# Performance work log

Hardware: AMD Instinct MI355X
Metric: run time of the kernel (lower is better)

## Reference

```python
import jax, jax.numpy as jnp
import numpy as np

# Static config matching init_kwargs
WZ, WH, WW = 2, 6, 12          # window size
MZ, MH, MW = 4, 16, 15          # ceil(input_shape / window_size) for (8,96,180)
HEADS, DIM, B = 6, 192, 1
DH = DIM // HEADS
P = WZ * WH * WW                # 144 tokens per window
WN = MZ * MH * MW               # 960 windows
WT = MZ * MH                    # 64 window types
SCALE = DH ** -0.5
TABLE = WZ * WZ * WH * WH * (2 * WW - 1)  # 3312 bias entries


def _position_index():
    zi = np.arange(WZ); zj = -np.arange(WZ) * WZ
    hi = np.arange(WH); hj = -np.arange(WH) * WH
    w = np.arange(WW)
    c1 = np.stack(np.meshgrid(zi, hi, w, indexing='ij')).reshape(3, -1)  # (3, P)
    c2 = np.stack(np.meshgrid(zj, hj, w, indexing='ij')).reshape(3, -1)  # (3, P)
    coords = (c1[:, :, None] - c2[:, None, :]).transpose(1, 2, 0)        # (P, P, 3)
    coords[:, :, 2] += WW - 1
    coords[:, :, 1] *= 2 * WW - 1
    coords[:, :, 0] *= (2 * WW - 1) * WH * WH
    return coords.sum(-1).reshape(-1)  # (P*P,)

POS_IDX = jnp.asarray(_position_index())


def setup_inputs() -> dict:
    key = jax.random.key(0)
    ks = jax.random.split(key, 5)
    x = jax.random.normal(ks[0], (B * WN, P, DIM), dtype=jnp.float32)
    mask = jnp.zeros((WN, P, P), dtype=jnp.float32)
    w_qkv = jax.random.normal(ks[1], (DIM, 3 * DIM), dtype=jnp.float32) * 0.02
    w_proj = jax.random.normal(ks[2], (DIM, DIM), dtype=jnp.float32) * 0.02
    b_proj = jnp.zeros((DIM,), dtype=jnp.float32)
    bias_table = jax.random.normal(ks[3], (TABLE, WT, HEADS), dtype=jnp.float32) * 0.02
    return {"x": x, "mask": mask, "w_qkv": w_qkv, "w_proj": w_proj,
            "b_proj": b_proj, "bias_table": bias_table}


def reference(x, mask, w_qkv, w_proj, b_proj, bias_table):
    BN = x.shape[0]  # B*WN
    qkv = (x @ w_qkv).reshape(BN, P, 3, HEADS, DH).transpose(2, 0, 3, 1, 4)  # (3,BN,h,P,dh)
    q, k, v = SCALE * qkv[0], qkv[1], qkv[2]
    attn = jnp.einsum('bhid,bhjd->bhij', q, k)  # (BN, h, P, P)
    # (B mZ mH mW) h P P -> (B mW) (mZ mH) h P P
    attn = attn.reshape(B, MZ, MH, MW, HEADS, P, P)
    attn = attn.transpose(0, 3, 1, 2, 4, 5, 6).reshape(B * MW, WT, HEADS, P, P)
    # gather earth-specific bias: (P*P, WT, h) -> (WT, h, P, P)
    bias = bias_table[POS_IDX].reshape(P, P, WT, HEADS).transpose(2, 3, 0, 1)
    attn = attn + bias  # broadcast over (B mW)
    # back to (B mZ mH mW) h P P
    attn = attn.reshape(B, MW, MZ, MH, HEADS, P, P)
    attn = attn.transpose(0, 2, 3, 1, 4, 5, 6).reshape(B, WN, HEADS, P, P)
    attn = attn + mask[None, :, None]  # (1, wN, 1, P, P)
    attn = jax.nn.softmax(attn, axis=-1).reshape(B * WN, HEADS, P, P)
    out = jnp.einsum('bhij,bhjd->bhid', attn, v)           # (BN, h, P, dh)
    out = out.transpose(0, 2, 1, 3).reshape(BN, P, DIM)    # merge heads
    return out @ w_proj + b_proj
```

## Files before the change

### kernel.cpp

```cpp
#include <hip/hip_runtime.h>

#define HEADS 6
#define DIM 192
#define DH 32
#define PW 144
#define WN 960
#define MWD 15
#define NTOK (WN*PW)
#define SCALE 0.17677669529663687f
#define LOG2E 1.4426950408889634f
#define SCALE2 (SCALE * LOG2E)

typedef __attribute__((ext_vector_type(8))) short bf16x8;
typedef __attribute__((ext_vector_type(4))) short bf16x4;
typedef __attribute__((ext_vector_type(4))) float f32x4;

#define MFMA16(a,b,c) __builtin_amdgcn_mfma_f32_16x16x32_bf16(a,b,c,0,0,0)

__device__ __forceinline__ unsigned short f2bf(float f) {
    unsigned int u = __builtin_bit_cast(unsigned int, f);
    u += 0x7fffu + ((u >> 16) & 1u);
    return (unsigned short)(u >> 16);
}
__device__ __forceinline__ float bf2f(unsigned short s) {
    unsigned int u = ((unsigned int)s) << 16;
    return __builtin_bit_cast(float, u);
}

__global__ __launch_bounds__(256) void prep_all(
        const float* __restrict__ x, const float* __restrict__ mask,
        const float* __restrict__ wqkv, const float* __restrict__ wproj,
        const float* __restrict__ btab,
        unsigned short* __restrict__ xb, unsigned short* __restrict__ bias_d,
        unsigned short* __restrict__ wqkvT, unsigned short* __restrict__ wprojT,
        int* __restrict__ flags) {
    __shared__ float shtab[3312];
    __shared__ int any;
    int b = blockIdx.x;
    if (b < 12960) {
        long long c = (long long)b * 256 + threadIdx.x;
        const float* p = x + c * 8;
        f32x4 v0 = *(const f32x4*)p;
        f32x4 v1 = *(const f32x4*)(p + 4);
        bf16x8 o;
        o[0] = (short)f2bf(v0[0]); o[1] = (short)f2bf(v0[1]);
        o[2] = (short)f2bf(v0[2]); o[3] = (short)f2bf(v0[3]);
        o[4] = (short)f2bf(v1[0]); o[5] = (short)f2bf(v1[1]);
        o[6] = (short)f2bf(v1[2]); o[7] = (short)f2bf(v1[3]);
        *(bf16x8*)(xb + c * 8) = o;
    } else if (b < 13344) {
        int b2 = b - 12960;
        int wt = b2 / 6, h = b2 % 6;
        for (int p = threadIdx.x; p < 3312; p += 256)
            shtab[p] = btab[p * 384 + wt * 6 + h] * LOG2E;
        __syncthreads();
        unsigned short* op = bias_d + (wt * 6 + h) * 20736;
        for (int c = threadIdx.x; c < 2592; c += 256) {
            int i = c / 18, j0 = (c % 18) * 8;
            int z1 = i / 72, h1 = (i / 12) % 6, w1 = i % 12;
            int pbase = z1 * 828 + h1 * 23 + w1 + 11;
            bf16x8 o;
            #pragma unroll
            for (int e = 0; e < 8; ++e) {
                int j = j0 + e;
                int z2 = j / 72, h2 = (j / 12) % 6, w2 = j % 12;
                int pos = pbase + z2 * 1656 + h2 * 138 - w2;
                o[e] = (short)f2bf(shtab[pos]);
            }
            *(bf16x8*)(op + i * 144 + j0) = o;
        }
    } else if (b < 14304) {
        int w = b - 13344;
        if (threadIdx.x == 0) any = 0;
        __syncthreads();
        const float* mp = mask + w * 20736;
        int nz = 0;
        for (int c = threadIdx.x; c < 5184; c += 256) {
            f32x4 v = *(const f32x4*)(mp + c * 4);
            if (v[0] != 0.f || v[1] != 0.f || v[2] != 0.f || v[3] != 0.f) nz = 1;
        }
        if (nz) atomicOr(&any, 1);
        __syncthreads();
        if (threadIdx.x == 0) flags[w] = any;
    } else {
        int t = (b - 14304) * 256 + threadIdx.x;
        if (t < 576 * 192) {
            int n = t / 192, k = t % 192;
            wqkvT[t] = f2bf(wqkv[k * 576 + n]);
        } else {
            int t2 = t - 576 * 192;
            int n = t2 / 192, k = t2 % 192;
            wprojT[t2] = f2bf(wproj[k * 192 + n]);
        }
    }
}

__global__ __launch_bounds__(256) void qkv_gemm(
        const unsigned short* __restrict__ xb, const unsigned short* __restrict__ wqkvT,
        unsigned short* __restrict__ qb, unsigned short* __restrict__ kb,
        unsigned short* __restrict__ vtb) {
    __shared__ unsigned short Bt[96 * 200];
    int bid = blockIdx.x;
    int r8 = bid & 7, s = bid >> 3;
    int nblk = s % 6;
    int mg = r8 * 45 + s / 6;
    int tid = threadIdx.x;
    int lane = tid & 63, wv = tid >> 6;
    int l16 = lane & 15, quad = lane >> 4;

    const unsigned short* wp = wqkvT + nblk * (96 * 192);
    #pragma unroll
    for (int it = 0; it < 9; ++it) {
        int c = tid + it * 256;
        int row = c / 24, c8 = (c % 24) * 8;
        *(bf16x8*)&Bt[row * 200 + c8] = *(const bf16x8*)(wp + c * 8);
    }
    __syncthreads();

    const unsigned short* Abase = xb + ((long long)mg * 6 * 64 + wv * 16 + l16) * 192
                                  + quad * 8;
    bf16x8 a0[6], a1[6];
    #pragma unroll
    for (int kc = 0; kc < 6; ++kc) a0[kc] = *(const bf16x8*)(Abase + kc * 32);

    #pragma unroll
    for (int t = 0; t < 6; ++t) {
        bf16x8* ac = (t & 1) ? a1 : a0;
        bf16x8* an = (t & 1) ? a0 : a1;
        if (t < 5) {
            const unsigned short* Anext = Abase + (long long)(t + 1) * (64 * 192);
            #pragma unroll
            for (int kc = 0; kc < 6; ++kc) an[kc] = *(const bf16x8*)(Anext + kc * 32);
        }
        f32x4 acc[6];
        #pragma unroll
        for (int i = 0; i < 6; ++i) acc[i] = (f32x4){0.f, 0.f, 0.f, 0.f};
        #pragma unroll
        for (int kc = 0; kc < 6; ++kc) {
            bf16x8 af = ac[kc];
            #pragma unroll
            for (int ct = 0; ct < 6; ++ct) {
                bf16x8 bfr = *(const bf16x8*)&Bt[(ct * 16 + l16) * 200 + kc * 32 + quad * 8];
                acc[ct] = MFMA16(af, bfr, acc[ct]);
            }
        }
        int mtile = mg * 6 + t;
        int token0 = mtile * 64 + wv * 16 + quad * 4;
        int win = token0 / 144;
        int p0 = token0 - win * 144;
        #pragma unroll
        for (int ct = 0; ct < 6; ++ct) {
            int c0 = nblk * 96 + ct * 16;
            int which = c0 / 192;
            int head = (c0 % 192) / 32;
            int d = (c0 % 32) + l16;
            if (which == 0) {
                int base = ((win * 6 + head) * 144 + p0) * 32 + d;
                #pragma unroll
                for (int r = 0; r < 4; ++r) qb[base + r * 32] = f2bf(acc[ct][r]);
            } else if (which == 1) {
                int base = ((win * 6 + head) * 144 + p0) * 32 + d;
                #pragma unroll
                for (int r = 0; r < 4; ++r) kb[base + r * 32] = f2bf(acc[ct][r]);
            } else {
                int base = ((win * 6 + head) * 32 + d) * 144 + p0;
                bf16x4 o;
                #pragma unroll
                for (int r = 0; r < 4; ++r) o[r] = (short)f2bf(acc[ct][r]);
                *(bf16x4*)&vtb[base] = o;
            }
        }
    }
}

__global__ __launch_bounds__(192, 3) void attn(
        const unsigned short* __restrict__ qb, const unsigned short* __restrict__ kb,
        const unsigned short* __restrict__ vtb, const unsigned short* __restrict__ bias_d,
        const float* __restrict__ mask, const int* __restrict__ mflags,
        unsigned short* __restrict__ Ob) {
    __shared__ unsigned short Kl[144 * 40];
    __shared__ unsigned short Vt[32 * 168];
    __shared__ unsigned short Pl[3 * 16 * 168];

    int bx = blockIdx.x;
    int r8 = bx & 7, s = bx >> 3;
    int h = s % 6;
    int win = r8 * 120 + s / 6;
    int wt = win / MWD;
    int tid = threadIdx.x;
    int lane = tid & 63, wv = tid >> 6;
    int l16 = lane & 15, quad = lane >> 4;

    int qoff = (win * 6 + h) * (144 * 32);
    #pragma unroll
    for (int it = 0; it < 3; ++it) {
        int c = tid + it * 192;
        int row = c >> 2, c8 = (c & 3) * 8;
        *(bf16x8*)&Kl[row * 40 + c8] = *(const bf16x8*)(kb + qoff + c * 8);
        int vr = c / 18, vc = (c % 18) * 8;
        *(bf16x8*)&Vt[vr * 168 + vc] = *(const bf16x8*)(vtb + qoff + c * 8);
    }
    bf16x8 qreg[3];
    #pragma unroll
    for (int rt = 0; rt < 3; ++rt)
        qreg[rt] = *(const bf16x8*)(qb + qoff + (((wv * 3 + rt) * 16) + l16) * 32 + quad * 8);
    {
        int row = lane >> 2, ch = lane & 3;
        *(bf16x4*)&Pl[wv * 2688 + row * 168 + 144 + ch * 4] = (bf16x4){0, 0, 0, 0};
    }
    if (tid < 96) {
        int row = tid / 3, off = 144 + (tid % 3) * 8;
        *(bf16x8*)&Vt[row * 168 + off] = (bf16x8){0, 0, 0, 0, 0, 0, 0, 0};
    }
    int mflag = mflags[win];
    __syncthreads();

    const float* maskp = mask + win * 20736;
    const unsigned short* biasp = bias_d + (wt * 6 + h) * 20736;
    const f32x4 z = {0.f, 0.f, 0.f, 0.f};
    int pb = wv * 2688;

    #pragma unroll
    for (int rt = 0; rt < 3; ++rt) {
        int i0 = (wv * 3 + rt) * 16;
        int ibase = (i0 + quad * 4) * 144 + l16;
        f32x4 bm[9];
        if (mflag) {
            #pragma unroll
            for (int ct = 0; ct < 9; ++ct) {
                #pragma unroll
                for (int r = 0; r < 4; ++r) {
                    int off = ibase + r * 144 + ct * 16;
                    bm[ct][r] = fmaf(maskp[off], LOG2E, bf2f(biasp[off]));
                }
            }
        } else {
            #pragma unroll
            for (int ct = 0; ct < 9; ++ct) {
                #pragma unroll
                for (int r = 0; r < 4; ++r) {
                    int off = ibase + r * 144 + ct * 16;
                    bm[ct][r] = bf2f(biasp[off]);
                }
            }
        }
        bf16x8 aq = qreg[rt];
        f32x4 sreg[9];
        #pragma unroll
        for (int ct = 0; ct < 9; ++ct) {
            bf16x8 bk = *(const bf16x8*)&Kl[(ct * 16 + l16) * 40 + quad * 8];
            sreg[ct] = MFMA16(aq, bk, z);
        }
        #pragma unroll
        for (int ct = 0; ct < 9; ++ct) {
            #pragma unroll
            for (int r = 0; r < 4; ++r)
                sreg[ct][r] = fmaf(sreg[ct][r], SCALE2, bm[ct][r]);
        }
        float inv[4];
        #pragma unroll
        for (int r = 0; r < 4; ++r) {
            float mx = sreg[0][r];
            #pragma unroll
            for (int ct = 1; ct < 9; ++ct) mx = fmaxf(mx, sreg[ct][r]);
            #pragma unroll
            for (int off = 1; off < 16; off <<= 1) mx = fmaxf(mx, __shfl_xor(mx, off, 64));
            float sum = 0.f;
            #pragma unroll
            for (int ct = 0; ct < 9; ++ct) {
                float e = __builtin_amdgcn_exp2f(sreg[ct][r] - mx);
                sreg[ct][r] = e; sum += e;
            }
            #pragma unroll
            for (int off = 1; off < 16; off <<= 1) sum += __shfl_xor(sum, off, 64);
            inv[r] = __builtin_amdgcn_rcpf(sum);
        }
        #pragma unroll
        for (int ct = 0; ct < 9; ++ct) {
            #pragma unroll
            for (int r = 0; r < 4; ++r)
                Pl[pb + (quad * 4 + r) * 168 + ct * 16 + l16] = f2bf(sreg[ct][r]);
        }
        f32x4 o0 = z, o1 = z;
        #pragma unroll
        for (int kc = 0; kc < 5; ++kc) {
            bf16x8 ap = *(const bf16x8*)&Pl[pb + l16 * 168 + kc * 32 + quad * 8];
            bf16x8 b0 = *(const bf16x8*)&Vt[l16 * 168 + kc * 32 + quad * 8];
            bf16x8 b1 = *(const bf16x8*)&Vt[(16 + l16) * 168 + kc * 32 + quad * 8];
            o0 = MFMA16(ap, b0, o0);
            o1 = MFMA16(ap, b1, o1);
        }
        #pragma unroll
        for (int r = 0; r < 4; ++r) {
            int i = i0 + quad * 4 + r;
            int ob = (win * 144 + i) * 192 + h * 32 + l16;
            Ob[ob] = f2bf(o0[r] * inv[r]);
            Ob[ob + 16] = f2bf(o1[r] * inv[r]);
        }
    }
}

__global__ __launch_bounds__(256) void out_gemm(
        const unsigned short* __restrict__ Ob, const unsigned short* __restrict__ wprojT,
        const float* __restrict__ bproj, float* __restrict__ out) {
    __shared__ unsigned short Bt[96 * 200];
    int bid = blockIdx.x;
    int r8 = bid & 7, s = bid >> 3;
    int nblk = s % 2;
    int mg = r8 * 45 + s / 2;
    int tid = threadIdx.x;
    int lane = tid & 63, wv = tid >> 6;
    int l16 = lane & 15, quad = lane >> 4;

    const unsigned short* wp = wprojT + nblk * (96 * 192);
    #pragma unroll
    for (int it = 0; it < 9; ++it) {
        int c = tid + it * 256;
        int row = c / 24, c8 = (c % 24) * 8;
        *(bf16x8*)&Bt[row * 200 + c8] = *(const bf16x8*)(wp + c * 8);
    }
    __syncthreads();

    const unsigned short* Abase = Ob + ((long long)mg * 6 * 64 + wv * 16 + l16) * 192
                                  + quad * 8;
    bf16x8 a0[6], a1[6];
    #pragma unroll
    for (int kc = 0; kc < 6; ++kc) a0[kc] = *(const bf16x8*)(Abase + kc * 32);

    #pragma unroll
    for (int t = 0; t < 6; ++t) {
        bf16x8* ac = (t & 1) ? a1 : a0;
        bf16x8* an = (t & 1) ? a0 : a1;
        if (t < 5) {
            const unsigned short* Anext = Abase + (long long)(t + 1) * (64 * 192);
            #pragma unroll
            for (int kc = 0; kc < 6; ++kc) an[kc] = *(const bf16x8*)(Anext + kc * 32);
        }
        f32x4 acc[6];
        #pragma unroll
        for (int i = 0; i < 6; ++i) acc[i] = (f32x4){0.f, 0.f, 0.f, 0.f};
        #pragma unroll
        for (int kc = 0; kc < 6; ++kc) {
            bf16x8 af = ac[kc];
            #pragma unroll
            for (int ct = 0; ct < 6; ++ct) {
                bf16x8 bfr = *(const bf16x8*)&Bt[(ct * 16 + l16) * 200 + kc * 32 + quad * 8];
                acc[ct] = MFMA16(af, bfr, acc[ct]);
            }
        }
        int token0 = (mg * 6 + t) * 64 + wv * 16 + quad * 4;
        #pragma unroll
        for (int ct = 0; ct < 6; ++ct) {
            int c = nblk * 96 + ct * 16 + l16;
            float bp = bproj[c];
            #pragma unroll
            for (int r = 0; r < 4; ++r)
                out[(token0 + r) * 192 + c] = acc[ct][r] + bp;
        }
    }
}

extern "C" void kernel_launch(void* const* d_in, const int* in_sizes, int n_in,
                              void* d_out, int out_size, void* d_ws, size_t ws_size,
                              hipStream_t stream) {
    const float* x     = (const float*)d_in[0];
    const float* mask  = (const float*)d_in[1];
    const float* wqkv  = (const float*)d_in[2];
    const float* wproj = (const float*)d_in[3];
    const float* bproj = (const float*)d_in[4];
    const float* btab  = (const float*)d_in[5];
    float* out = (float*)d_out;
    int* mflags = (int*)d_out;

    char* ws = (char*)d_ws;
    unsigned short* xb     = (unsigned short*)(ws + 0);
    unsigned short* Ob     = (unsigned short*)(ws + 0);
    unsigned short* qb     = (unsigned short*)(ws + 53084160);
    unsigned short* kb     = (unsigned short*)(ws + 106168320);
    unsigned short* vtb    = (unsigned short*)(ws + 159252480);
    unsigned short* bias_d = (unsigned short*)(ws + 212336640);
    unsigned short* wqkvT  = (unsigned short*)(ws + 228261888);
    unsigned short* wprojT = (unsigned short*)(ws + 228483072);

    prep_all<<<14880, 256, 0, stream>>>(x, mask, wqkv, wproj, btab,
                                        xb, bias_d, wqkvT, wprojT, mflags);
    qkv_gemm<<<2160, 256, 0, stream>>>(xb, wqkvT, qb, kb, vtb);
    attn<<<5760, 192, 0, stream>>>(qb, kb, vtb, bias_d, mask, mflags, Ob);
    out_gemm<<<720, 256, 0, stream>>>(Ob, wprojT, bproj, out);
}
```

Baseline: 443.0 us.

## Fuse fp32-to-bf16 conversion of x into QKV GEMM A-tile load

Removes the separate x-conversion pass from the prep kernel and has each QKV GEMM block load and convert its own 64-row fp32 tile of x into LDS. The GEMM is restructured so each block covers all 576 output columns, streaming weight fragments from global memory with double buffering instead of staging them in LDS. This avoids writing and re-reading a bf16 copy of x, at the cost of more global or L2 weight reads per block and a longer serial MFMA loop.

```diff
diff --git a/kernel.cpp b/kernel.cpp
--- a/kernel.cpp
+++ b/kernel.cpp
@@ -28,29 +28,17 @@
 }
 
 __global__ __launch_bounds__(256) void prep_all(
-        const float* __restrict__ x, const float* __restrict__ mask,
+        const float* __restrict__ mask,
         const float* __restrict__ wqkv, const float* __restrict__ wproj,
         const float* __restrict__ btab,
-        unsigned short* __restrict__ xb, unsigned short* __restrict__ bias_d,
+        unsigned short* __restrict__ bias_d,
         unsigned short* __restrict__ wqkvT, unsigned short* __restrict__ wprojT,
         int* __restrict__ flags) {
     __shared__ float shtab[3312];
     __shared__ int any;
     int b = blockIdx.x;
-    if (b < 12960) {
-        long long c = (long long)b * 256 + threadIdx.x;
-        const float* p = x + c * 8;
-        f32x4 v0 = *(const f32x4*)p;
-        f32x4 v1 = *(const f32x4*)(p + 4);
-        bf16x8 o;
-        o[0] = (short)f2bf(v0[0]); o[1] = (short)f2bf(v0[1]);
-        o[2] = (short)f2bf(v0[2]); o[3] = (short)f2bf(v0[3]);
-        o[4] = (short)f2bf(v1[0]); o[5] = (short)f2bf(v1[1]);
-        o[6] = (short)f2bf(v1[2]); o[7] = (short)f2bf(v1[3]);
-        *(bf16x8*)(xb + c * 8) = o;
-    } else if (b < 13344) {
-        int b2 = b - 12960;
-        int wt = b2 / 6, h = b2 % 6;
+    if (b < 384) {
+        int wt = b / 6, h = b % 6;
         for (int p = threadIdx.x; p < 3312; p += 256)
             shtab[p] = btab[p * 384 + wt * 6 + h] * LOG2E;
         __syncthreads();
@@ -69,8 +57,8 @@
             }
             *(bf16x8*)(op + i * 144 + j0) = o;
         }
-    } else if (b < 14304) {
-        int w = b - 13344;
+    } else if (b < 1344) {
+        int w = b - 384;
         if (threadIdx.x == 0) any = 0;
         __syncthreads();
         const float* mp = mask + w * 20736;
@@ -83,7 +71,7 @@
         __syncthreads();
         if (threadIdx.x == 0) flags[w] = any;
     } else {
-        int t = (b - 14304) * 256 + threadIdx.x;
+        int t = (b - 1344) * 256 + threadIdx.x;
         if (t < 576 * 192) {
             int n = t / 192, k = t % 192;
             wqkvT[t] = f2bf(wqkv[k * 576 + n]);
@@ -96,79 +84,80 @@
 }
 
 __global__ __launch_bounds__(256) void qkv_gemm(
-        const unsigned short* __restrict__ xb, const unsigned short* __restrict__ wqkvT,
+        const float* __restrict__ x, const unsigned short* __restrict__ wqkvT,
         unsigned short* __restrict__ qb, unsigned short* __restrict__ kb,
         unsigned short* __restrict__ vtb) {
-    __shared__ unsigned short Bt[96 * 200];
+    __shared__ unsigned short A[64 * 200];
     int bid = blockIdx.x;
-    int r8 = bid & 7, s = bid >> 3;
-    int nblk = s % 6;
-    int mg = r8 * 45 + s / 6;
+    int mtile = (bid & 7) * 270 + (bid >> 3);
     int tid = threadIdx.x;
     int lane = tid & 63, wv = tid >> 6;
     int l16 = lane & 15, quad = lane >> 4;
 
-    const unsigned short* wp = wqkvT + nblk * (96 * 192);
-    #pragma unroll
-    for (int it = 0; it < 9; ++it) {
+    const float* xp = x + (long long)mtile * (64 * 192);
+    #pragma unroll
+    for (int it = 0; it < 6; ++it) {
         int c = tid + it * 256;
         int row = c / 24, c8 = (c % 24) * 8;
-        *(bf16x8*)&Bt[row * 200 + c8] = *(const bf16x8*)(wp + c * 8);
+        const float* p = xp + c * 8;
+        f32x4 v0 = *(const f32x4*)p;
+        f32x4 v1 = *(const f32x4*)(p + 4);
+        bf16x8 o;
+        o[0] = (short)f2bf(v0[0]); o[1] = (short)f2bf(v0[1]);
+        o[2] = (short)f2bf(v0[2]); o[3] = (short)f2bf(v0[3]);
+        o[4] = (short)f2bf(v1[0]); o[5] = (short)f2bf(v1[1]);
+        o[6] = (short)f2bf(v1[2]); o[7] = (short)f2bf(v1[3]);
+        *(bf16x8*)&A[row * 200 + c8] = o;
     }
     __syncthreads();
 
-    const unsigned short* Abase = xb + ((long long)mg * 6 * 64 + wv * 16 + l16) * 192
-                                  + quad * 8;
-    bf16x8 a0[6], a1[6];
-    #pragma unroll
-    for (int kc = 0; kc < 6; ++kc) a0[kc] = *(const bf16x8*)(Abase + kc * 32);
-
-    #pragma unroll
-    for (int t = 0; t < 6; ++t) {
-        bf16x8* ac = (t & 1) ? a1 : a0;
-        bf16x8* an = (t & 1) ? a0 : a1;
-        if (t < 5) {
-            const unsigned short* Anext = Abase + (long long)(t + 1) * (64 * 192);
-            #pragma unroll
-            for (int kc = 0; kc < 6; ++kc) an[kc] = *(const bf16x8*)(Anext + kc * 32);
-        }
-        f32x4 acc[6];
-        #pragma unroll
-        for (int i = 0; i < 6; ++i) acc[i] = (f32x4){0.f, 0.f, 0.f, 0.f};
-        #pragma unroll
-        for (int kc = 0; kc < 6; ++kc) {
-            bf16x8 af = ac[kc];
-            #pragma unroll
-            for (int ct = 0; ct < 6; ++ct) {
-                bf16x8 bfr = *(const bf16x8*)&Bt[(ct * 16 + l16) * 200 + kc * 32 + quad * 8];
-                acc[ct] = MFMA16(af, bfr, acc[ct]);
-            }
-        }
-        int mtile = mg * 6 + t;
-        int token0 = mtile * 64 + wv * 16 + quad * 4;
-        int win = token0 / 144;
-        int p0 = token0 - win * 144;
-        #pragma unroll
-        for (int ct = 0; ct < 6; ++ct) {
-            int c0 = nblk * 96 + ct * 16;
-            int which = c0 / 192;
-            int head = (c0 % 192) / 32;
-            int d = (c0 % 32) + l16;
-            if (which == 0) {
-                int base = ((win * 6 + head) * 144 + p0) * 32 + d;
-                #pragma unroll
-                for (int r = 0; r < 4; ++r) qb[base + r * 32] = f2bf(acc[ct][r]);
-            } else if (which == 1) {
-                int base = ((win * 6 + head) * 144 + p0) * 32 + d;
-                #pragma unroll
-                for (int r = 0; r < 4; ++r) kb[base + r * 32] = f2bf(acc[ct][r]);
-            } else {
-                int base = ((win * 6 + head) * 32 + d) * 144 + p0;
-                bf16x4 o;
-                #pragma unroll
-                for (int r = 0; r < 4; ++r) o[r] = (short)f2bf(acc[ct][r]);
-                *(bf16x4*)&vtb[base] = o;
-            }
+    bf16x8 a[6];
+    #pragma unroll
+    for (int kc = 0; kc < 6; ++kc)
+        a[kc] = *(const bf16x8*)&A[(wv * 16 + l16) * 200 + kc * 32 + quad * 8];
+
+    int token0 = mtile * 64 + wv * 16 + quad * 4;
+    int win = token0 / 144;
+    int p0 = token0 - win * 144;
+
+    const unsigned short* Bbase = wqkvT + l16 * 192 + quad * 8;
+    const f32x4 z = {0.f, 0.f, 0.f, 0.f};
+
+    bf16x8 b0[6], b1[6];
+    #pragma unroll
+    for (int kc = 0; kc < 6; ++kc) b0[kc] = *(const bf16x8*)(Bbase + kc * 32);
+
+    #pragma unroll
+    for (int cb = 0; cb < 36; ++cb) {
+        bf16x8* bc = (cb & 1) ? b1 : b0;
+        bf16x8* bn = (cb & 1) ? b0 : b1;
+        if (cb < 35) {
+            const unsigned short* Bn = Bbase + (cb + 1) * (16 * 192);
+            #pragma unroll
+            for (int kc = 0; kc < 6; ++kc) bn[kc] = *(const bf16x8*)(Bn + kc * 32);
+        }
+        f32x4 acc = z;
+        #pragma unroll
+        for (int kc = 0; kc < 6; ++kc) acc = MFMA16(a[kc], bc[kc], acc);
+
+        int c0 = cb * 16;
+        int which = c0 / 192;
+        int head = (c0 % 192) / 32;
+        int d = (c0 % 32) + l16;
+        if (which == 0) {
+            int base = ((win * 6 + head) * 144 + p0) * 32 + d;
+            #pragma unroll
+            for (int r = 0; r < 4; ++r) qb[base + r * 32] = f2bf(acc[r]);
+        } else if (which == 1) {
+            int base = ((win * 6 + head) * 144 + p0) * 32 + d;
+            #pragma unroll
+            for (int r = 0; r < 4; ++r) kb[base + r * 32] = f2bf(acc[r]);
+        } else {
+            int base = ((win * 6 + head) * 32 + d) * 144 + p0;
+            bf16x4 o;
+            #pragma unroll
+            for (int r = 0; r < 4; ++r) o[r] = (short)f2bf(acc[r]);
+            *(bf16x4*)&vtb[base] = o;
         }
     }
 }
@@ -373,7 +362,6 @@
     int* mflags = (int*)d_out;
 
     char* ws = (char*)d_ws;
-    unsigned short* xb     = (unsigned short*)(ws + 0);
     unsigned short* Ob     = (unsigned short*)(ws + 0);
     unsigned short* qb     = (unsigned short*)(ws + 53084160);
     unsigned short* kb     = (unsigned short*)(ws + 106168320);
@@ -382,9 +370,9 @@
     unsigned short* wqkvT  = (unsigned short*)(ws + 228261888);
     unsigned short* wprojT = (unsigned short*)(ws + 228483072);
 
-    prep_all<<<14880, 256, 0, stream>>>(x, mask, wqkv, wproj, btab,
-                                        xb, bias_d, wqkvT, wprojT, mflags);
-    qkv_gemm<<<2160, 256, 0, stream>>>(xb, wqkvT, qb, kb, vtb);
+    prep_all<<<1920, 256, 0, stream>>>(mask, wqkv, wproj, btab,
+                                       bias_d, wqkvT, wprojT, mflags);
+    qkv_gemm<<<2160, 256, 0, stream>>>(x, wqkvT, qb, kb, vtb);
     attn<<<5760, 192, 0, stream>>>(qb, kb, vtb, bias_d, mask, mflags, Ob);
     out_gemm<<<720, 256, 0, stream>>>(Ob, wprojT, bproj, out);
 }
```

Result: slower. 572.7 us (+29.3%).
